# Kernel optimization log

Measured on AMD Instinct MI355X. Metric: run time of the kernel, lower is better.

Reference implementation:

```python
import jax, jax.numpy as jnp
import numpy as np

B, S, D = 2, 1024, 1024
E, K, I = 8, 2, 1024
LIMIT = 7.0
ALPHA = 1.702


def setup_inputs() -> dict:
    key = jax.random.key(0)
    k0, k1, k2, k3 = jax.random.split(key, 4)
    return {
        "x": jax.random.normal(k0, (B, S, D), jnp.float32),
        "norm_w": jnp.ones((D,), jnp.float32),
        "gate_w": jax.random.normal(k1, (E, D), jnp.float32) / np.sqrt(D).astype(np.float32),
        "gate_b": jnp.zeros((E,), jnp.float32),
        "mlp1_w": jax.random.normal(k2, (E, 2 * I, D), jnp.float32) / np.sqrt(D).astype(np.float32),
        "mlp1_b": jnp.zeros((E, 2 * I), jnp.float32),
        "mlp2_w": jax.random.normal(k3, (E, D, I), jnp.float32) / np.sqrt(I).astype(np.float32),
        "mlp2_b": jnp.zeros((E, D), jnp.float32),
    }


def _swiglu(t, limit):
    # interleaved gate/linear split (gpt-oss style) with clamping
    glu = jnp.minimum(t[..., ::2], limit)
    lin = jnp.clip(t[..., 1::2], -limit, limit)
    return glu * jax.nn.sigmoid(ALPHA * glu) * (lin + 1.0)


def reference(x, norm_w, gate_w, gate_b, mlp1_w, mlp1_b, mlp2_w, mlp2_b):
    eps = jnp.finfo(x.dtype).eps
    # RMSNorm
    h = x * jax.lax.rsqrt(jnp.mean(x * x, axis=-1, keepdims=True) + eps) * norm_w
    flat = h.reshape(-1, D)                              # [T, D]
    # top-k gating
    logits = flat @ gate_w.T + gate_b                    # [T, E]
    vals, idx = jax.lax.top_k(logits, K)                 # sorted descending
    wts = jax.nn.softmax(vals, axis=-1)                  # [T, K]
    # per-expert SwiGLU MLP (dense over experts, identical math to per-token gather)
    t1 = jnp.einsum('td,efd->tef', flat, mlp1_w) + mlp1_b   # [T, E, 2I]
    act = _swiglu(t1, LIMIT)                                 # [T, E, I]
    y = jnp.einsum('tei,edi->ted', act, mlp2_w) + mlp2_b     # [T, E, D]
    # gather selected experts and combine
    sel = jnp.take_along_axis(y, idx[:, :, None], axis=1)    # [T, K, D]
    out = jnp.sum(sel * wts[:, :, None], axis=1).reshape(x.shape)
    return x + out
```

## Files before the change

kernel.cpp:

```cpp
#include <hip/hip_runtime.h>
#include <stdint.h>

#define TNUM 2048
#define DDIM 1024
#define NEXP 8
#define KSEL 2
#define IDIM 1024
#define TWOI 2048
#define LIMITV 7.0f
#define ALPHAV 1.702f
#define ROWT_MAX 40

typedef __attribute__((ext_vector_type(8))) short bf16x8;
typedef __attribute__((ext_vector_type(4))) float f32x4;

__device__ __forceinline__ unsigned short f2bf(float f) {
  unsigned u = __float_as_uint(f);
  u += 0x7FFF + ((u >> 16) & 1);
  return (unsigned short)(u >> 16);
}

__device__ __forceinline__ int4 cvt8(float4 a, float4 b) {
  union { unsigned short us[8]; int4 v; } o;
  o.us[0] = f2bf(a.x); o.us[1] = f2bf(a.y); o.us[2] = f2bf(a.z); o.us[3] = f2bf(a.w);
  o.us[4] = f2bf(b.x); o.us[5] = f2bf(b.y); o.us[6] = f2bf(b.z); o.us[7] = f2bf(b.w);
  return o.v;
}

__device__ __forceinline__ void gl2lds16(const void* g, void* l) {
  __builtin_amdgcn_global_load_lds(
      (__attribute__((address_space(1))) unsigned int*)(uintptr_t)g,
      (__attribute__((address_space(3))) unsigned int*)(uintptr_t)l, 16, 0, 0);
}

__device__ __forceinline__ int xcd_swz(int bid, int total) {
  int q = total >> 3, r = total & 7;
  int xcd = bid & 7, pos = bid >> 3;
  return (xcd < r ? xcd * (q + 1) : r * (q + 1) + (xcd - r) * q) + pos;
}

__global__ __launch_bounds__(256) void k_cvt(const float* __restrict__ src,
                                             unsigned short* __restrict__ dst, int n8) {
  int i = blockIdx.x * blockDim.x + threadIdx.x;
  if (i >= n8) return;
  const float4* s = (const float4*)src;
  float4 a = s[2 * i], b = s[2 * i + 1];
  ((int4*)dst)[i] = cvt8(a, b);
}

__global__ __launch_bounds__(256) void k_rms_gate(
    const float* __restrict__ x, const float* __restrict__ norm_w,
    const float* __restrict__ gate_w, const float* __restrict__ gate_b,
    unsigned short* __restrict__ hb, int* __restrict__ tidx,
    float* __restrict__ twt) {
  const int lane = threadIdx.x & 63;
  const int t = blockIdx.x * 4 + (threadIdx.x >> 6);

  const float4* xr  = (const float4*)x + (size_t)t * 256 + lane * 4;
  const float4* nwr = (const float4*)norm_w + lane * 4;
  const float4* gbr = (const float4*)gate_b;
  float4 xv[4], nwv[4];
#pragma unroll
  for (int i = 0; i < 4; ++i) xv[i] = xr[i];
  float4 gb0 = gbr[0], gb1 = gbr[1];
#pragma unroll
  for (int i = 0; i < 4; ++i) nwv[i] = nwr[i];

  float ss = 0.f;
#pragma unroll
  for (int i = 0; i < 4; ++i)
    ss += xv[i].x * xv[i].x + xv[i].y * xv[i].y + xv[i].z * xv[i].z + xv[i].w * xv[i].w;
#pragma unroll
  for (int m = 1; m < 64; m <<= 1) ss += __shfl_xor(ss, m);
  const float sc = rsqrtf(ss * (1.0f / DDIM) + 1.1920929e-07f);

  float4 h[4];
#pragma unroll
  for (int i = 0; i < 4; ++i) {
    h[i].x = xv[i].x * sc * nwv[i].x;
    h[i].y = xv[i].y * sc * nwv[i].y;
    h[i].z = xv[i].z * sc * nwv[i].z;
    h[i].w = xv[i].w * sc * nwv[i].w;
  }
  int4* hw = (int4*)(hb + (size_t)t * DDIM + lane * 16);
  hw[0] = cvt8(h[0], h[1]);
  hw[1] = cvt8(h[2], h[3]);

  float p[NEXP];
#pragma unroll
  for (int e = 0; e < NEXP; ++e) {
    const float4* g4 = (const float4*)gate_w + e * 256 + lane * 4;
    float4 a = g4[0], b = g4[1], c = g4[2], d = g4[3];
    p[e] = h[0].x * a.x + h[0].y * a.y + h[0].z * a.z + h[0].w * a.w
         + h[1].x * b.x + h[1].y * b.y + h[1].z * b.z + h[1].w * b.w
         + h[2].x * c.x + h[2].y * c.y + h[2].z * c.z + h[2].w * c.w
         + h[3].x * d.x + h[3].y * d.y + h[3].z * d.z + h[3].w * d.w;
  }
#pragma unroll
  for (int m = 1; m < 64; m <<= 1) {
#pragma unroll
    for (int e = 0; e < NEXP; ++e) p[e] += __shfl_xor(p[e], m);
  }
  p[0] += gb0.x; p[1] += gb0.y; p[2] += gb0.z; p[3] += gb0.w;
  p[4] += gb1.x; p[5] += gb1.y; p[6] += gb1.z; p[7] += gb1.w;

  if (lane == 0) {
    int i0 = 0; float v0 = p[0];
#pragma unroll
    for (int e = 1; e < NEXP; ++e) if (p[e] > v0) { v0 = p[e]; i0 = e; }
    int i1 = -1; float v1 = -3.4e38f;
#pragma unroll
    for (int e = 0; e < NEXP; ++e) if (e != i0 && p[e] > v1) { v1 = p[e]; i1 = e; }
    float e1 = __expf(v1 - v0);
    float w0 = 1.f / (1.f + e1);
    int2 ip; ip.x = i0; ip.y = i1;
    float2 wp; wp.x = w0; wp.y = e1 * w0;
    ((int2*)tidx)[t] = ip;
    ((float2*)twt)[t] = wp;
  }
}

__global__ __launch_bounds__(256) void k_sched(
    const int* __restrict__ tidx, int* __restrict__ meta,
    int* __restrict__ tl, int* __restrict__ rows, int* __restrict__ sof) {
  __shared__ int cur[NEXP];
  __shared__ int off[NEXP];
  const int tid = threadIdx.x;
  if (tid < NEXP) cur[tid] = 0;
  __syncthreads();
  int e_[16], rel_[16];
#pragma unroll
  for (int k = 0; k < 16; ++k) {
    int i = tid * 16 + k;
    int e = tidx[i];
    e_[k] = e;
    rel_[k] = atomicAdd(&cur[e], 1);
  }
  __syncthreads();
  if (tid == 0) {
    int acc = 0, nt = 0;
    for (int e = 0; e < NEXP; ++e) {
      meta[8 + e] = acc; off[e] = acc;
      int c = cur[e]; acc += c;
      int ntile = (c + 127) >> 7;
      for (int r = 0; r < ntile; ++r) tl[nt++] = (e << 8) | r;
    }
    meta[16] = acc;
    meta[25] = nt;
  }
  __syncthreads();
#pragma unroll
  for (int k = 0; k < 16; ++k) {
    int i = tid * 16 + k;
    int slot = off[e_[k]] + rel_[k];
    rows[slot] = i >> 1;
    sof[i] = slot;
  }
}

__global__ __launch_bounds__(256, 2) void k_gemm1(
    const unsigned short* __restrict__ hb, const unsigned short* __restrict__ w1b,
    const float* __restrict__ mlp1_b, const int* __restrict__ meta,
    const int* __restrict__ tl, const int* __restrict__ rows,
    unsigned short* __restrict__ actb) {
  const int nt = meta[25];
  const int total = nt * (TWOI / 128);
  const int bid = blockIdx.x;
  if (bid >= total) return;
  const int j = xcd_swz(bid, total);
  const int ct = j / nt;
  const int tile = tl[j - ct * nt];
  const int e = tile >> 8, rt = tile & 255;
  const int offs = meta[8 + e];
  const int n_e = meta[9 + e] - offs;
  const int tid = threadIdx.x, lane = tid & 63, wid = tid >> 6;

  __shared__ unsigned short As[2][128][64];
  __shared__ unsigned short Bs[2][128][64];
  __shared__ int srow[128];
  if (tid < 128) srow[tid] = rows[offs + min(rt * 128 + tid, n_e - 1)];
  __syncthreads();

  const int rloc = tid >> 3;
  const int csw  = (((tid & 7) ^ (rloc & 7)) << 3);
  const unsigned short* gA[4];
  const unsigned short* gB[4];
  const unsigned short* w1e = w1b + (size_t)e * TWOI * DDIM;
#pragma unroll
  for (int jj = 0; jj < 4; ++jj) {
    gA[jj] = hb + (size_t)srow[jj * 32 + rloc] * DDIM + csw;
    gB[jj] = w1e + (size_t)(ct * 128 + jj * 32 + rloc) * DDIM + csw;
  }

#define G1_STAGE(BUF, KT)                                                      \
  _Pragma("unroll") for (int jj = 0; jj < 4; ++jj) {                           \
    gl2lds16(gA[jj] + (KT) * 64, &As[BUF][0][0] + jj * 2048 + tid * 8);        \
    gl2lds16(gB[jj] + (KT) * 64, &Bs[BUF][0][0] + jj * 2048 + tid * 8);        \
  }

  f32x4 acc[4][4];
#pragma unroll
  for (int m = 0; m < 4; ++m)
#pragma unroll
    for (int n = 0; n < 4; ++n) acc[m][n] = (f32x4){0.f, 0.f, 0.f, 0.f};

  const int wr = wid >> 1, wc = wid & 1;
  const int lrow = lane & 15, ksub = (lane >> 4) * 8;
  const int NK = DDIM / 64;

  G1_STAGE(0, 0)
  __syncthreads();

  int cur = 0;
  for (int kt = 0; kt < NK; ++kt) {
    if (kt + 1 < NK) { G1_STAGE(cur ^ 1, kt + 1) }
#pragma unroll
    for (int kk = 0; kk < 2; ++kk) {
      bf16x8 af[4], bfr[4];
#pragma unroll
      for (int m = 0; m < 4; ++m) {
        int row = wr * 64 + m * 16 + lrow;
        int chunk = ((kk * 32 + ksub) >> 3) ^ (row & 7);
        af[m] = *(const bf16x8*)&As[cur][row][chunk * 8];
      }
#pragma unroll
      for (int n = 0; n < 4; ++n) {
        int row = wc * 64 + n * 16 + lrow;
        int chunk = ((kk * 32 + ksub) >> 3) ^ (row & 7);
        bfr[n] = *(const bf16x8*)&Bs[cur][row][chunk * 8];
      }
#pragma unroll
      for (int m = 0; m < 4; ++m)
#pragma unroll
        for (int n = 0; n < 4; ++n)
          acc[m][n] = __builtin_amdgcn_mfma_f32_16x16x32_bf16(af[m], bfr[n], acc[m][n], 0, 0, 0);
    }
    __syncthreads();
    cur ^= 1;
  }
#undef G1_STAGE

  const float* b1e = mlp1_b + e * TWOI;
#pragma unroll
  for (int m = 0; m < 4; ++m) {
#pragma unroll
    for (int n = 0; n < 4; ++n) {
      int cg = ct * 128 + wc * 64 + n * 16 + (lane & 15);
      float bias = b1e[cg];
#pragma unroll
      for (int j2 = 0; j2 < 4; ++j2) {
        float val = acc[m][n][j2] + bias;
        float part = __shfl_xor(val, 1);
        int rl = wr * 64 + m * 16 + ((lane >> 4) << 2) + j2;
        if (!(lane & 1)) {
          float glu = fminf(val, LIMITV);
          float lin = fminf(fmaxf(part, -LIMITV), LIMITV);
          float s = 1.f / (1.f + __expf(-ALPHAV * glu));
          float a = glu * s * (lin + 1.f);
          if (rt * 128 + rl < n_e)
            actb[(size_t)(offs + rt * 128 + rl) * IDIM + (cg >> 1)] = f2bf(a);
        }
      }
    }
  }
}

__global__ __launch_bounds__(256, 2) void k_gemm2(
    const unsigned short* __restrict__ actb, const unsigned short* __restrict__ w2b,
    const float* __restrict__ mlp2_b, const int* __restrict__ meta,
    const int* __restrict__ tl, float* __restrict__ ybuf) {
  const int nt = meta[25];
  const int total = nt * (DDIM / 128);
  const int bid = blockIdx.x;
  if (bid >= total) return;
  const int j = xcd_swz(bid, total);
  const int ct = j / nt;
  const int tile = tl[j - ct * nt];
  const int e = tile >> 8, rt = tile & 255;
  const int offs = meta[8 + e];
  const int n_e = meta[9 + e] - offs;
  const int tid = threadIdx.x, lane = tid & 63, wid = tid >> 6;

  __shared__ unsigned short As[2][128][64];
  __shared__ unsigned short Bs[2][128][64];

  const int rloc = tid >> 3;
  const int csw  = (((tid & 7) ^ (rloc & 7)) << 3);
  const unsigned short* gA[4];
  const unsigned short* gB[4];
  const unsigned short* w2e = w2b + (size_t)e * DDIM * IDIM;
#pragma unroll
  for (int jj = 0; jj < 4; ++jj) {
    gA[jj] = actb + (size_t)(offs + min(rt * 128 + jj * 32 + rloc, n_e - 1)) * IDIM + csw;
    gB[jj] = w2e + (size_t)(ct * 128 + jj * 32 + rloc) * IDIM + csw;
  }

#define G2_STAGE(BUF, KT)                                                      \
  _Pragma("unroll") for (int jj = 0; jj < 4; ++jj) {                           \
    gl2lds16(gA[jj] + (KT) * 64, &As[BUF][0][0] + jj * 2048 + tid * 8);        \
    gl2lds16(gB[jj] + (KT) * 64, &Bs[BUF][0][0] + jj * 2048 + tid * 8);        \
  }

  f32x4 acc[4][4];
#pragma unroll
  for (int m = 0; m < 4; ++m)
#pragma unroll
    for (int n = 0; n < 4; ++n) acc[m][n] = (f32x4){0.f, 0.f, 0.f, 0.f};

  const int wr = wid >> 1, wc = wid & 1;
  const int lrow = lane & 15, ksub = (lane >> 4) * 8;
  const int NK = IDIM / 64;

  G2_STAGE(0, 0)
  __syncthreads();

  int cur = 0;
  for (int kt = 0; kt < NK; ++kt) {
    if (kt + 1 < NK) { G2_STAGE(cur ^ 1, kt + 1) }
#pragma unroll
    for (int kk = 0; kk < 2; ++kk) {
      bf16x8 af[4], bfr[4];
#pragma unroll
      for (int m = 0; m < 4; ++m) {
        int row = wr * 64 + m * 16 + lrow;
        int chunk = ((kk * 32 + ksub) >> 3) ^ (row & 7);
        af[m] = *(const bf16x8*)&As[cur][row][chunk * 8];
      }
#pragma unroll
      for (int n = 0; n < 4; ++n) {
        int row = wc * 64 + n * 16 + lrow;
        int chunk = ((kk * 32 + ksub) >> 3) ^ (row & 7);
        bfr[n] = *(const bf16x8*)&Bs[cur][row][chunk * 8];
      }
#pragma unroll
      for (int m = 0; m < 4; ++m)
#pragma unroll
        for (int n = 0; n < 4; ++n)
          acc[m][n] = __builtin_amdgcn_mfma_f32_16x16x32_bf16(af[m], bfr[n], acc[m][n], 0, 0, 0);
    }
    __syncthreads();
    cur ^= 1;
  }
#undef G2_STAGE

  const float* b2e = mlp2_b + e * DDIM;
#pragma unroll
  for (int m = 0; m < 4; ++m) {
#pragma unroll
    for (int n = 0; n < 4; ++n) {
      int d = ct * 128 + wc * 64 + n * 16 + (lane & 15);
      float bias = b2e[d];
#pragma unroll
      for (int j2 = 0; j2 < 4; ++j2) {
        int rl = wr * 64 + m * 16 + ((lane >> 4) << 2) + j2;
        if (rt * 128 + rl < n_e)
          ybuf[(size_t)(offs + rt * 128 + rl) * DDIM + d] = acc[m][n][j2] + bias;
      }
    }
  }
}

__global__ __launch_bounds__(256) void k_combine(
    const float* __restrict__ x, const float* __restrict__ ybuf,
    const int* __restrict__ sof, const float* __restrict__ twt,
    float* __restrict__ out) {
  int t = blockIdx.x, tid = threadIdx.x;
  int s0 = sof[2 * t], s1 = sof[2 * t + 1];
  float w0 = twt[2 * t], w1 = twt[2 * t + 1];
  float4 xv = ((const float4*)x)[t * 256 + tid];
  float4 y0 = ((const float4*)ybuf)[(size_t)s0 * 256 + tid];
  float4 y1 = ((const float4*)ybuf)[(size_t)s1 * 256 + tid];
  float4 o;
  o.x = xv.x + w0 * y0.x + w1 * y1.x;
  o.y = xv.y + w0 * y0.y + w1 * y1.y;
  o.z = xv.z + w0 * y0.z + w1 * y1.z;
  o.w = xv.w + w0 * y0.w + w1 * y1.w;
  ((float4*)out)[t * 256 + tid] = o;
}

extern "C" void kernel_launch(void* const* d_in, const int* in_sizes, int n_in,
                              void* d_out, int out_size, void* d_ws, size_t ws_size,
                              hipStream_t stream) {
  const float* x      = (const float*)d_in[0];
  const float* norm_w = (const float*)d_in[1];
  const float* gate_w = (const float*)d_in[2];
  const float* gate_b = (const float*)d_in[3];
  const float* mlp1_w = (const float*)d_in[4];
  const float* mlp1_b = (const float*)d_in[5];
  const float* mlp2_w = (const float*)d_in[6];
  const float* mlp2_b = (const float*)d_in[7];
  float* out = (float*)d_out;

  char* w = (char*)d_ws;
  unsigned short* w1b = (unsigned short*)w; w += (size_t)NEXP * TWOI * DDIM * 2;
  unsigned short* w2b = (unsigned short*)w; w += (size_t)NEXP * DDIM * IDIM * 2;
  unsigned short* hb  = (unsigned short*)w; w += (size_t)TNUM * DDIM * 2;
  unsigned short* actb = (unsigned short*)w; w += (size_t)TNUM * KSEL * IDIM * 2;
  float* ybuf = (float*)w; w += (size_t)TNUM * KSEL * DDIM * 4;
  int*   tidx = (int*)w;  w += TNUM * KSEL * 4;
  float* twt  = (float*)w; w += TNUM * KSEL * 4;
  int*   sof  = (int*)w;  w += TNUM * KSEL * 4;
  int*   rows = (int*)w;  w += TNUM * KSEL * 4;
  int*   meta = (int*)w;  w += 32 * 4;
  int*   tl   = (int*)w;  w += 64 * 4;

  k_cvt<<<(NEXP * DDIM * IDIM / 8 + 255) / 256, 256, 0, stream>>>(mlp2_w, w2b, NEXP * DDIM * IDIM / 8);
  k_cvt<<<(NEXP * TWOI * DDIM / 8 + 255) / 256, 256, 0, stream>>>(mlp1_w, w1b, NEXP * TWOI * DDIM / 8);
  k_rms_gate<<<TNUM / 4, 256, 0, stream>>>(x, norm_w, gate_w, gate_b, hb, tidx, twt);
  k_sched<<<1, 256, 0, stream>>>(tidx, meta, tl, rows, sof);
  k_gemm1<<<dim3(ROWT_MAX * (TWOI / 128)), 256, 0, stream>>>(hb, w1b, mlp1_b, meta, tl, rows, actb);
  k_gemm2<<<dim3(ROWT_MAX * (DDIM / 128)), 256, 0, stream>>>(actb, w2b, mlp2_b, meta, tl, ybuf);
  k_combine<<<TNUM, 256, 0, stream>>>(x, ybuf, sof, twt, out);
}
```

Measured before the change: 112.7 us.

## Overlap next-tile loads with MFMA via vmcnt waits and merge weight conversion kernels

The GEMM main loops now issue the next tile's global-to-LDS loads and then wait only for the older batch (vmcnt(8)) before a raw barrier. Previously __syncthreads drained all outstanding loads, so the prefetch was not truly overlapped with compute. The loops are also fully unrolled with a compile-time buffer index. Separately, the two fp32-to-bf16 weight conversion launches are merged into one kernel to save a launch. The hand-written waitcnt relies on the compiler's instruction ordering and count assumptions, which is a correctness risk.

```diff
diff --git a/kernel.cpp b/kernel.cpp
--- a/kernel.cpp
+++ b/kernel.cpp
@@ -14,6 +14,10 @@
 typedef __attribute__((ext_vector_type(8))) short bf16x8;
 typedef __attribute__((ext_vector_type(4))) float f32x4;
 
+#define VMCNT8() asm volatile("s_waitcnt vmcnt(8)" ::: "memory")
+#define VMCNT0() asm volatile("s_waitcnt vmcnt(0)" ::: "memory")
+#define BARRIER() asm volatile("s_barrier" ::: "memory")
+
 __device__ __forceinline__ unsigned short f2bf(float f) {
   unsigned u = __float_as_uint(f);
   u += 0x7FFF + ((u >> 16) & 1);
@@ -39,13 +43,17 @@
   return (xcd < r ? xcd * (q + 1) : r * (q + 1) + (xcd - r) * q) + pos;
 }
 
-__global__ __launch_bounds__(256) void k_cvt(const float* __restrict__ src,
-                                             unsigned short* __restrict__ dst, int n8) {
+__global__ __launch_bounds__(256) void k_cvt2(
+    const float* __restrict__ w1, const float* __restrict__ w2,
+    unsigned short* __restrict__ d1, unsigned short* __restrict__ d2,
+    int n81, int n8tot) {
   int i = blockIdx.x * blockDim.x + threadIdx.x;
-  if (i >= n8) return;
-  const float4* s = (const float4*)src;
-  float4 a = s[2 * i], b = s[2 * i + 1];
-  ((int4*)dst)[i] = cvt8(a, b);
+  if (i >= n8tot) return;
+  const float4* s; int4* d; int k;
+  if (i < n81) { s = (const float4*)w1; d = (int4*)d1; k = i; }
+  else         { s = (const float4*)w2; d = (int4*)d2; k = i - n81; }
+  float4 a = s[2 * k], b = s[2 * k + 1];
+  d[k] = cvt8(a, b);
 }
 
 __global__ __launch_bounds__(256) void k_rms_gate(
@@ -209,11 +217,16 @@
   const int NK = DDIM / 64;
 
   G1_STAGE(0, 0)
-  __syncthreads();
-
-  int cur = 0;
+#pragma unroll
   for (int kt = 0; kt < NK; ++kt) {
-    if (kt + 1 < NK) { G1_STAGE(cur ^ 1, kt + 1) }
+    const int cur = kt & 1;
+    if (kt + 1 < NK) {
+      G1_STAGE(cur ^ 1, kt + 1)
+      VMCNT8();
+    } else {
+      VMCNT0();
+    }
+    BARRIER();
 #pragma unroll
     for (int kk = 0; kk < 2; ++kk) {
       bf16x8 af[4], bfr[4];
@@ -235,8 +248,7 @@
         for (int n = 0; n < 4; ++n)
           acc[m][n] = __builtin_amdgcn_mfma_f32_16x16x32_bf16(af[m], bfr[n], acc[m][n], 0, 0, 0);
     }
-    __syncthreads();
-    cur ^= 1;
+    BARRIER();
   }
 #undef G1_STAGE
 
@@ -312,11 +324,16 @@
   const int NK = IDIM / 64;
 
   G2_STAGE(0, 0)
-  __syncthreads();
-
-  int cur = 0;
+#pragma unroll
   for (int kt = 0; kt < NK; ++kt) {
-    if (kt + 1 < NK) { G2_STAGE(cur ^ 1, kt + 1) }
+    const int cur = kt & 1;
+    if (kt + 1 < NK) {
+      G2_STAGE(cur ^ 1, kt + 1)
+      VMCNT8();
+    } else {
+      VMCNT0();
+    }
+    BARRIER();
 #pragma unroll
     for (int kk = 0; kk < 2; ++kk) {
       bf16x8 af[4], bfr[4];
@@ -338,8 +355,7 @@
         for (int n = 0; n < 4; ++n)
           acc[m][n] = __builtin_amdgcn_mfma_f32_16x16x32_bf16(af[m], bfr[n], acc[m][n], 0, 0, 0);
     }
-    __syncthreads();
-    cur ^= 1;
+    BARRIER();
   }
 #undef G2_STAGE
 
@@ -404,8 +420,9 @@
   int*   meta = (int*)w;  w += 32 * 4;
   int*   tl   = (int*)w;  w += 64 * 4;
 
-  k_cvt<<<(NEXP * DDIM * IDIM / 8 + 255) / 256, 256, 0, stream>>>(mlp2_w, w2b, NEXP * DDIM * IDIM / 8);
-  k_cvt<<<(NEXP * TWOI * DDIM / 8 + 255) / 256, 256, 0, stream>>>(mlp1_w, w1b, NEXP * TWOI * DDIM / 8);
+  const int n81 = NEXP * TWOI * DDIM / 8;
+  const int n8tot = n81 + NEXP * DDIM * IDIM / 8;
+  k_cvt2<<<(n8tot + 255) / 256, 256, 0, stream>>>(mlp1_w, mlp2_w, w1b, w2b, n81, n8tot);
   k_rms_gate<<<TNUM / 4, 256, 0, stream>>>(x, norm_w, gate_w, gate_b, hb, tidx, twt);
   k_sched<<<1, 256, 0, stream>>>(tidx, meta, tl, rows, sof);
   k_gemm1<<<dim3(ROWT_MAX * (TWOI / 128)), 256, 0, stream>>>(hb, w1b, mlp1_b, meta, tl, rows, actb);
```

Measured after the change: 110.7 us. Within noise of the previous version (-1.8%).
